# Performance work log

Hardware: AMD Instinct MI355X
Metric: run time of the kernel (lower is better)

## Reference

```python
import jax, jax.numpy as jnp
import numpy as np


def _d2(a, b):
    # squared euclidean distances, clamped at 0 (matches _full_cdist before sqrt)
    a2 = jnp.sum(a * a, axis=1)[:, None]
    b2 = jnp.sum(b * b, axis=1)[None, :]
    return jnp.clip(a2 + b2 - 2.0 * (a @ b.T), 0.0, None)


def _node_weights(pts, w1, b1, w2, b2):
    h = jax.nn.relu(pts @ w1 + b1)
    logits = h @ w2 + b2
    w = jax.nn.softplus(logits) + 1e-6
    w = w / jnp.sum(w)
    return w[:, 0]


def setup_inputs() -> dict:
    key = jax.random.key(0)
    ks = jax.random.split(key, 8)
    N, M, D, H, S = 8192, 8192, 2, 32, 3
    return {
        "base_points": jax.random.normal(ks[0], (N, D), jnp.float32),
        "target_points": jax.random.normal(ks[1], (M, D), jnp.float32),
        "log_sigmas": jnp.log(jnp.array([0.05, 0.1, 0.2], jnp.float32)),
        "log_scale": 0.1 * jax.random.normal(ks[2], (D,), jnp.float32),
        "wn_w1": jax.random.normal(ks[3], (D, H), jnp.float32) / np.sqrt(D),
        "wn_b1": jnp.zeros((H,), jnp.float32),
        "wn_w2": jax.random.normal(ks[4], (H, 1), jnp.float32) / np.sqrt(H),
        "wn_b2": jnp.zeros((1,), jnp.float32),
        "g_w1": jax.random.normal(ks[5], (4, H), jnp.float32) / 2.0,
        "g_b1": jnp.zeros((H,), jnp.float32),
        "g_w2": jax.random.normal(ks[6], (H, S), jnp.float32) / np.sqrt(H),
        "g_b2": jnp.zeros((S,), jnp.float32),
        "bias": jnp.zeros((1,), jnp.float32),
    }


def reference(base_points, target_points, log_sigmas, log_scale,
              wn_w1, wn_b1, wn_w2, wn_b2,
              g_w1, g_b1, g_w2, g_b2, bias):
    # learned anisotropic per-axis scale
    scale = jnp.exp(log_scale)
    base = base_points * scale
    target = target_points * scale

    # learned positive, normalized node weights (shared weight_net)
    w_b = _node_weights(base, wn_w1, wn_b1, wn_w2, wn_b2)
    w_t = _node_weights(target, wn_w1, wn_b1, wn_w2, wn_b2)

    # kde_mmd_loss with center=True: subtract weighted mean of each cloud.
    bc = base - jnp.sum(w_b[:, None] * base, axis=0)
    tc = target - jnp.sum(w_t[:, None] * target, axis=0)

    # squared distances computed ONCE, reused across all sigma bands
    d2_aa = _d2(bc, bc)
    d2_bb = _d2(tc, tc)
    d2_ab = _d2(bc, tc)

    sigmas = jnp.exp(log_sigmas)

    def band_loss(sigma):
        inv = 1.0 / (2.0 * sigma * sigma)
        kaa = jnp.exp(-d2_aa * inv)
        kbb = jnp.exp(-d2_bb * inv)
        kab = jnp.exp(-d2_ab * inv)
        # weighted MMD^2: w_a K_aa w_a + w_b K_bb w_b - 2 w_a K_ab w_b
        return (w_b @ (kaa @ w_b) + w_t @ (kbb @ w_t)
                - 2.0 * (w_b @ (kab @ w_t)))

    per_band = jnp.stack([band_loss(sigmas[i]) for i in range(sigmas.shape[0])])

    # gating statistics (torch.tensor([...]) detaches -> stop_gradient)
    dist = jnp.sqrt(_d2(base, target))
    mean_dist = jnp.mean(dist)
    var_dist = jnp.var(dist, ddof=1)  # torch .var() is unbiased
    n_base = base_points.shape[0]
    size_diff = abs(float(n_base - target_points.shape[0])) / (n_base + 1e-6)
    weight_var = jnp.var(w_b, ddof=1) + jnp.var(w_t, ddof=1)
    stats = jax.lax.stop_gradient(
        jnp.stack([mean_dist, var_dist,
                   jnp.asarray(size_diff, base.dtype), weight_var]))

    mix_logits = jax.nn.relu(stats @ g_w1 + g_b1) @ g_w2 + g_b2
    gw = jax.nn.softplus(mix_logits)
    gw = gw / jnp.sum(gw)
    return jnp.sum(gw * per_band) + bias[0]
```

## Files before the change

### kernel.cpp

```cpp
#include <hip/hip_runtime.h>
#include <math.h>

#define JT 64
#define ITILE 1024
#define T8 8
#define NJOB_AB 1024
#define NJOB_TRI 576
#define NBLK (NJOB_AB + 2 * NJOB_TRI)
#define L2E 1.4426950408889634f

typedef float v2f __attribute__((ext_vector_type(2)));

__device__ inline float fexp2n(float x) {
  float r;
  asm("v_exp_f32 %0, -%1" : "=v"(r) : "v"(x));
  return r;
}
__device__ inline float fsqrt(float x) {
  float r;
  asm("v_sqrt_f32 %0, %1" : "=v"(r) : "v"(x));
  return r;
}

__device__ inline double wred_d(double v) {
#pragma unroll
  for (int o = 32; o > 0; o >>= 1) v += __shfl_down(v, o, 64);
  return v;
}

__device__ inline double bred(double v, double* sm) {
  v = wred_d(v);
  __syncthreads();
  if ((threadIdx.x & 63) == 0) sm[threadIdx.x >> 6] = v;
  __syncthreads();
  return sm[0] + sm[1] + sm[2] + sm[3];
}

__device__ inline void slot_reduce(const double* slot, double* smean) {
  if (threadIdx.x < 64) {
    int l = threadIdx.x;
    const double* sl = slot + l * 4;
#pragma unroll
    for (int c = 0; c < 4; ++c) {
      double v = sl[c];
      double vb = (l < 32) ? v : 0.0;
      double vt = (l < 32) ? 0.0 : v;
      vb = wred_d(vb);
      vt = wred_d(vt);
      if (l == 0) {
        smean[c] = vb;
        smean[4 + c] = vt;
      }
    }
  }
}

__global__ __launch_bounds__(256) void prep_kernel(
    const float* __restrict__ base, const float* __restrict__ target,
    const float* __restrict__ log_sigmas, const float* __restrict__ log_scale,
    const float* __restrict__ w1, const float* __restrict__ b1,
    const float* __restrict__ w2, const float* __restrict__ b2,
    float2* __restrict__ pxy, float* __restrict__ pu,
    double* __restrict__ slot, unsigned* __restrict__ fctr, int n) {
  __shared__ double sm[4];
  int gid = blockIdx.x * 256 + threadIdx.x;
  int isT = gid >= n;
  const float* pts = isT ? target : base;
  int idx = isT ? gid - n : gid;
  float ex = __expf(log_scale[0]);
  float ey = __expf(log_scale[1]);
  float s2 = __expf(log_sigmas[2]);
  float r2 = __fsqrt_rn(L2E / (2.f * s2 * s2));
  float2 p = ((const float2*)pts)[idx];
  float xr = p.x * ex, yr = p.y * ey;
  float logit = b2[0];
#pragma unroll
  for (int k = 0; k < 32; ++k) {
    float h = fmaf(xr, w1[k], fmaf(yr, w1[32 + k], b1[k]));
    h = fmaxf(h, 0.f);
    logit = fmaf(h, w2[k], logit);
  }
  float u = fmaxf(logit, 0.f) + log1pf(__expf(-fabsf(logit))) + 1e-6f;
  float X = xr * r2, Y = yr * r2;
  pxy[gid] = make_float2(X, Y);
  pu[gid] = u;
  double su = bred((double)u, sm);
  double qu = bred((double)u * (double)u, sm);
  double mx = bred((double)u * (double)X, sm);
  double my = bred((double)u * (double)Y, sm);
  if (threadIdx.x == 0) {
    double* s = slot + blockIdx.x * 4;
    s[0] = su;
    s[1] = qu;
    s[2] = mx;
    s[3] = my;
    if (blockIdx.x == 0) *fctr = 0u;
  }
}

template <bool AB, bool FAST>
__device__ inline void tile_loop(const float* sx, const float* sy,
                                 const float* su, const float* snb,
                                 const v2f xi2[4], const v2f yi2[4],
                                 const v2f al2[4], float rr0, float rr1,
                                 v2f a0[4], v2f a1[4], v2f a2[4], float& sdo,
                                 float& sqo) {
  float sda = 0.f, sdb = 0.f;
  v2f sq2 = {0.f, 0.f};
  const v2f vz = {0.f, 0.f};
#pragma unroll 2
  for (int jj = 0; jj < JT / 2; ++jj) {
    v2f xj = *(const v2f*)&sx[2 * jj];
    v2f yj = *(const v2f*)&sy[2 * jj];
    v2f uj = *(const v2f*)&su[2 * jj];
    v2f nbj;
    if constexpr (AB) nbj = *(const v2f*)&snb[2 * jj];
#pragma unroll
    for (int i = 0; i < 4; ++i) {
      v2f dx = xi2[i] - xj;
      v2f dy = yi2[i] - yj;
      v2f pos = dx * dx + dy * dy;
      v2f k2 = {fexp2n(pos.x), fexp2n(pos.y)};
      v2f k0, k1;
      if constexpr (FAST) {
        v2f t = k2 * k2;
        k1 = t * t;
        v2f t1 = k1 * k1;
        k0 = t1 * t1;
      } else {
        v2f m1 = pos * rr1;
        v2f m0 = pos * rr0;
        k1 = {fexp2n(m1.x), fexp2n(m1.y)};
        k0 = {fexp2n(m0.x), fexp2n(m0.y)};
      }
      a0[i] += uj * k0;
      a1[i] += uj * k1;
      a2[i] += uj * k2;
      if constexpr (AB) {
        v2f anb = al2[i] + nbj;
        v2f d2u = pos + anb;
        d2u = __builtin_elementwise_max(d2u, vz);
        sq2 += d2u;
        sda += fsqrt(d2u.x);
        sdb += fsqrt(d2u.y);
      }
    }
  }
  sdo = sda + sdb;
  sqo = sq2.x + sq2.y;
}

__global__ __launch_bounds__(256) void pair_kernel(
    const float2* __restrict__ pxy, const float* __restrict__ pu,
    const double* __restrict__ slot, double* __restrict__ paa,
    double* __restrict__ pbb, double* __restrict__ pab,
    double* __restrict__ psd, double* __restrict__ psq,
    unsigned* __restrict__ fctr, const float* __restrict__ log_sigmas,
    const float* __restrict__ g_w1, const float* __restrict__ g_b1,
    const float* __restrict__ g_w2, const float* __restrict__ g_b2,
    const float* __restrict__ bias, float* __restrict__ out, int n) {
  __shared__ __align__(16) float sx[JT];
  __shared__ __align__(16) float sy[JT];
  __shared__ __align__(16) float su[JT];
  __shared__ __align__(16) float snb[JT];
  __shared__ double sm[4];
  __shared__ double smean[8];
  __shared__ int lastf;

  int b = blockIdx.x;
  int m, it, jt = 0, j0, pidx;
  if (b < NJOB_AB) {
    m = 2;
    pidx = b;
    it = b >> 7;
    j0 = (b & 127) * JT;
  } else {
    int r = b - NJOB_AB;
    m = (r < NJOB_TRI) ? 0 : 1;
    if (m == 1) r -= NJOB_TRI;
    pidx = r;
    int tile = r >> 4;
    int q = r & 15;
    int idx = tile, len = T8;
    it = 0;
    while (idx >= len) {
      idx -= len;
      --len;
      ++it;
    }
    jt = it + idx;
    j0 = jt * ITILE + q * JT;
  }
  const float2* pxyI = pxy + ((m == 1) ? n : 0);
  const float* puI = pu + ((m == 1) ? n : 0);
  const float2* pxyJ = pxy + ((m == 0) ? 0 : n);
  const float* puJ = pu + ((m == 0) ? 0 : n);

  float cx = 0.f, cy = 0.f, cx2 = 0.f, cy2 = 0.f, cc = 0.f;
  if (m == 2) {
    slot_reduce(slot, smean);
  }

  float s0 = __expf(log_sigmas[0]);
  float s1 = __expf(log_sigmas[1]);
  float s2 = __expf(log_sigmas[2]);
  float rr0 = (s2 * s2) / (s0 * s0);
  float rr1 = (s2 * s2) / (s1 * s1);
  bool fast = (fabsf(rr0 - 16.f) <= 0.016f) && (fabsf(rr1 - 4.f) <= 0.004f);

  if (m == 2) {
    __syncthreads();
    cx = (float)(smean[2] / smean[0] - smean[6] / smean[4]);
    cy = (float)(smean[3] / smean[0] - smean[7] / smean[4]);
    cx2 = 2.f * cx;
    cy2 = 2.f * cy;
    cc = cx * cx + cy * cy;
  }

  if (threadIdx.x < JT) {
    float2 v = pxyJ[j0 + threadIdx.x];
    sx[threadIdx.x] = v.x;
    sy[threadIdx.x] = v.y;
    su[threadIdx.x] = puJ[j0 + threadIdx.x];
    if (m == 2) snb[threadIdx.x] = -fmaf(cx2, v.x, cy2 * v.y);
  }
  __syncthreads();

  int i0 = it * ITILE + threadIdx.x;
  v2f xi2[4], yi2[4], al2[4];
  float u[4];
#pragma unroll
  for (int i = 0; i < 4; ++i) {
    float2 P = pxyI[i0 + i * 256];
    u[i] = puI[i0 + i * 256];
    float xv = P.x, yv = P.y, alv = 0.f;
    if (m == 2) {
      xv -= cx;
      yv -= cy;
      alv = fmaf(cx2, xv, cy2 * yv) + cc;
    }
    xi2[i] = (v2f){xv, xv};
    yi2[i] = (v2f){yv, yv};
    al2[i] = (v2f){alv, alv};
  }

  v2f a0[4] = {}, a1[4] = {}, a2[4] = {};
  float sd = 0.f, sq = 0.f;
  if (m == 2) {
    if (fast)
      tile_loop<true, true>(sx, sy, su, snb, xi2, yi2, al2, rr0, rr1, a0, a1,
                            a2, sd, sq);
    else
      tile_loop<true, false>(sx, sy, su, snb, xi2, yi2, al2, rr0, rr1, a0, a1,
                             a2, sd, sq);
  } else {
    if (fast)
      tile_loop<false, true>(sx, sy, su, snb, xi2, yi2, al2, rr0, rr1, a0, a1,
                             a2, sd, sq);
    else
      tile_loop<false, false>(sx, sy, su, snb, xi2, yi2, al2, rr0, rr1, a0,
                              a1, a2, sd, sq);
  }

  double wgt = (m != 2 && jt != it) ? 2.0 : 1.0;
  double c0 = 0.0, c1 = 0.0, c2 = 0.0;
#pragma unroll
  for (int i = 0; i < 4; ++i) {
    c0 += (double)u[i] * (double)(a0[i].x + a0[i].y);
    c1 += (double)u[i] * (double)(a1[i].x + a1[i].y);
    c2 += (double)u[i] * (double)(a2[i].x + a2[i].y);
  }
  double r0 = bred(c0, sm) * wgt;
  double r1 = bred(c1, sm) * wgt;
  double r2d = bred(c2, sm) * wgt;
  double* prow = (m == 0) ? paa : (m == 1) ? pbb : pab;
  int stride = (m == 2) ? NJOB_AB : NJOB_TRI;
  if (threadIdx.x == 0) {
    prow[0 * stride + pidx] = r0;
    prow[1 * stride + pidx] = r1;
    prow[2 * stride + pidx] = r2d;
  }
  if (m == 2) {
    double rsd = bred((double)sd, sm);
    double rsq = bred((double)sq, sm);
    if (threadIdx.x == 0) {
      psd[pidx] = rsd;
      psq[pidx] = rsq;
    }
  }

  if (threadIdx.x == 0) {
    __threadfence();
    unsigned old = atomicAdd(fctr, 1u);
    lastf = (old == NBLK - 1) ? 1 : 0;
  }
  __syncthreads();
  if (!lastf) return;
  __threadfence();

  slot_reduce(slot, smean);
  __syncthreads();
  int t = threadIdx.x;
  double vaa[3], vbb[3], vab[3];
  for (int s = 0; s < 3; ++s) {
    const double* pa = paa + s * NJOB_TRI;
    const double* pb = pbb + s * NJOB_TRI;
    const double* pc = pab + s * NJOB_AB;
    double va = pa[t] + pa[t + 256] + ((t < 64) ? pa[t + 512] : 0.0);
    double vb = pb[t] + pb[t + 256] + ((t < 64) ? pb[t + 512] : 0.0);
    double vc = pc[t] + pc[t + 256] + pc[t + 512] + pc[t + 768];
    vaa[s] = bred(va, sm);
    vbb[s] = bred(vb, sm);
    vab[s] = bred(vc, sm);
  }
  double sdt = bred(psd[t] + psd[t + 256] + psd[t + 512] + psd[t + 768], sm);
  double sqt = bred(psq[t] + psq[t + 256] + psq[t + 512] + psq[t + 768], sm);

  if (threadIdx.x == 0) {
    double Sb = smean[0], Qb = smean[1], St = smean[4], Qt = smean[5];
    double pband[3];
    for (int s = 0; s < 3; ++s)
      pband[s] = vaa[s] / (Sb * Sb) + vbb[s] / (St * St) -
                 2.0 * vab[s] / (Sb * St);
    double s2d = (double)s2;
    double r2sq = (double)L2E / (2.0 * s2d * s2d);
    double sd_real = sdt / sqrt(r2sq);
    double sq_real = sqt / r2sq;
    double NN = (double)n;
    double NM = NN * NN;
    double mean_d = sd_real / NM;
    double var_d = (sq_real - sd_real * sd_real / NM) / (NM - 1.0);
    double wv = (Qb / (Sb * Sb) - 1.0 / NN) / (NN - 1.0) +
                (Qt / (St * St) - 1.0 / NN) / (NN - 1.0);
    float st[4] = {(float)mean_d, (float)var_d, 0.f, (float)wv};
    float gl[3] = {g_b2[0], g_b2[1], g_b2[2]};
    for (int k = 0; k < 32; ++k) {
      float h = g_b1[k];
      for (int c = 0; c < 4; ++c) h = fmaf(st[c], g_w1[c * 32 + k], h);
      h = fmaxf(h, 0.f);
      for (int s = 0; s < 3; ++s) gl[s] = fmaf(h, g_w2[k * 3 + s], gl[s]);
    }
    float gw[3];
    float gsum = 0.f;
    for (int s = 0; s < 3; ++s) {
      gw[s] = fmaxf(gl[s], 0.f) + log1pf(__expf(-fabsf(gl[s])));
      gsum += gw[s];
    }
    double r = 0.0;
    for (int s = 0; s < 3; ++s) r += (double)(gw[s] / gsum) * pband[s];
    out[0] = (float)(r + (double)bias[0]);
  }
}

extern "C" void kernel_launch(void* const* d_in, const int* in_sizes, int n_in,
                              void* d_out, int out_size, void* d_ws,
                              size_t ws_size, hipStream_t stream) {
  const float* base = (const float*)d_in[0];
  const float* target = (const float*)d_in[1];
  const float* log_sigmas = (const float*)d_in[2];
  const float* log_scale = (const float*)d_in[3];
  const float* wn_w1 = (const float*)d_in[4];
  const float* wn_b1 = (const float*)d_in[5];
  const float* wn_w2 = (const float*)d_in[6];
  const float* wn_b2 = (const float*)d_in[7];
  const float* g_w1 = (const float*)d_in[8];
  const float* g_b1 = (const float*)d_in[9];
  const float* g_w2 = (const float*)d_in[10];
  const float* g_b2 = (const float*)d_in[11];
  const float* bias = (const float*)d_in[12];
  int n = in_sizes[0] / 2;

  double* dbase = (double*)d_ws;
  double* slot = dbase;
  double* paa = dbase + 256;
  double* pbb = paa + 3 * NJOB_TRI;
  double* pab = pbb + 3 * NJOB_TRI;
  double* psd = pab + 3 * NJOB_AB;
  double* psq = psd + NJOB_AB;
  double* dend = psq + NJOB_AB;
  float2* pxy = (float2*)dend;
  float* pu = (float*)(pxy + 2 * n);
  unsigned* fctr = (unsigned*)(pu + 2 * n);

  prep_kernel<<<(2 * n) / 256, 256, 0, stream>>>(
      base, target, log_sigmas, log_scale, wn_w1, wn_b1, wn_w2, wn_b2, pxy, pu,
      slot, fctr, n);
  pair_kernel<<<NBLK, 256, 0, stream>>>(pxy, pu, slot, paa, pbb, pab, psd, psq,
                                        fctr, log_sigmas, g_w1, g_b1, g_w2,
                                        g_b2, bias, (float*)d_out, n);
}
```

Before: 148.7 us.

## Expand pair distances algebraically, use packed FP32 ops, and compute squared-distance sum analytically

The inner pair loop now expands distances as |xi|^2 - 2 xi·xj + |xj|^2 using hand-written v_pk_fma/v_pk_add/v_pk_mul with op_sel broadcasts. The j-tile is packed as a float4 (x, y, |x|^2, u) in shared memory. The sum of squared cross distances is derived in closed form from per-cloud moments collected in prep, which removes the per-pair accumulation and its extra reduction. Blocks drop to 128 threads, each holding 8 i-points in packed pairs. The expanded form can lose precision through cancellation, and the closed-form sum skips the clamp at zero.

```diff
diff --git a/kernel.cpp b/kernel.cpp
--- a/kernel.cpp
+++ b/kernel.cpp
@@ -11,15 +11,58 @@
 
 typedef float v2f __attribute__((ext_vector_type(2)));
 
-__device__ inline float fexp2n(float x) {
-  float r;
-  asm("v_exp_f32 %0, -%1" : "=v"(r) : "v"(x));
-  return r;
-}
-__device__ inline float fsqrt(float x) {
-  float r;
-  asm("v_sqrt_f32 %0, %1" : "=v"(r) : "v"(x));
-  return r;
+__device__ inline v2f pk_add(v2f a, v2f b) {
+  v2f d;
+  asm("v_pk_add_f32 %0, %1, %2" : "=v"(d) : "v"(a), "v"(b));
+  return d;
+}
+__device__ inline v2f pk_mul(v2f a, v2f b) {
+  v2f d;
+  asm("v_pk_mul_f32 %0, %1, %2" : "=v"(d) : "v"(a), "v"(b));
+  return d;
+}
+__device__ inline v2f pk_fma_bh_bl(v2f a, v2f b, v2f c) {
+  v2f d;
+  asm("v_pk_fma_f32 %0, %1, %2, %3 op_sel:[0,1,0] op_sel_hi:[1,1,0]"
+      : "=v"(d) : "v"(a), "v"(b), "v"(c));
+  return d;
+}
+__device__ inline v2f pk_fma_bl(v2f a, v2f b, v2f c) {
+  v2f d;
+  asm("v_pk_fma_f32 %0, %1, %2, %3 op_sel:[0,0,0] op_sel_hi:[1,0,1]"
+      : "=v"(d) : "v"(a), "v"(b), "v"(c));
+  return d;
+}
+__device__ inline void pk_acc_bh(v2f& acc, v2f a, v2f b) {
+  asm("v_pk_fma_f32 %0, %1, %2, %0 op_sel:[0,1,0] op_sel_hi:[1,1,1]"
+      : "+v"(acc) : "v"(a), "v"(b));
+}
+__device__ inline void pk_accp(v2f& acc, v2f a) {
+  asm("v_pk_add_f32 %0, %1, %0" : "+v"(acc) : "v"(a));
+}
+__device__ inline v2f pk_add_bl(v2f a, v2f b) {
+  v2f d;
+  asm("v_pk_add_f32 %0, %1, %2 op_sel:[0,0] op_sel_hi:[1,0]"
+      : "=v"(d) : "v"(a), "v"(b));
+  return d;
+}
+__device__ inline v2f pk_add_bh(v2f a, v2f b) {
+  v2f d;
+  asm("v_pk_add_f32 %0, %1, %2 op_sel:[0,1] op_sel_hi:[1,1]"
+      : "=v"(d) : "v"(a), "v"(b));
+  return d;
+}
+__device__ inline v2f pexpn(v2f p) {
+  float lo, hi;
+  asm("v_exp_f32 %0, -%1" : "=v"(lo) : "v"(p.x));
+  asm("v_exp_f32 %0, -%1" : "=v"(hi) : "v"(p.y));
+  return (v2f){lo, hi};
+}
+__device__ inline v2f psqrta(v2f p) {
+  float lo, hi;
+  asm("v_sqrt_f32 %0, abs(%1)" : "=v"(lo) : "v"(p.x));
+  asm("v_sqrt_f32 %0, abs(%1)" : "=v"(hi) : "v"(p.y));
+  return (v2f){lo, hi};
 }
 
 __device__ inline double wred_d(double v) {
@@ -28,20 +71,23 @@
   return v;
 }
 
-__device__ inline double bred(double v, double* sm) {
+template <int NW>
+__device__ inline double bredN(double v, double* sm) {
   v = wred_d(v);
   __syncthreads();
   if ((threadIdx.x & 63) == 0) sm[threadIdx.x >> 6] = v;
   __syncthreads();
-  return sm[0] + sm[1] + sm[2] + sm[3];
-}
-
-__device__ inline void slot_reduce(const double* slot, double* smean) {
+  double r = sm[0];
+#pragma unroll
+  for (int w = 1; w < NW; ++w) r += sm[w];
+  return r;
+}
+
+__device__ inline void slot_reduce(const double* slot, double* smean, int nc) {
   if (threadIdx.x < 64) {
     int l = threadIdx.x;
-    const double* sl = slot + l * 4;
-#pragma unroll
-    for (int c = 0; c < 4; ++c) {
+    const double* sl = slot + l * 8;
+    for (int c = 0; c < nc; ++c) {
       double v = sl[c];
       double vb = (l < 32) ? v : 0.0;
       double vt = (l < 32) ? 0.0 : v;
@@ -49,7 +95,7 @@
       vt = wred_d(vt);
       if (l == 0) {
         smean[c] = vb;
-        smean[4 + c] = vt;
+        smean[8 + c] = vt;
       }
     }
   }
@@ -84,87 +130,94 @@
   float X = xr * r2, Y = yr * r2;
   pxy[gid] = make_float2(X, Y);
   pu[gid] = u;
-  double su = bred((double)u, sm);
-  double qu = bred((double)u * (double)u, sm);
-  double mx = bred((double)u * (double)X, sm);
-  double my = bred((double)u * (double)Y, sm);
+  double su = bredN<4>((double)u, sm);
+  double qu = bredN<4>((double)u * (double)u, sm);
+  double mx = bredN<4>((double)u * (double)X, sm);
+  double my = bredN<4>((double)u * (double)Y, sm);
+  double sx = bredN<4>((double)X, sm);
+  double sy = bredN<4>((double)Y, sm);
+  double sr = bredN<4>((double)X * (double)X + (double)Y * (double)Y, sm);
   if (threadIdx.x == 0) {
-    double* s = slot + blockIdx.x * 4;
+    double* s = slot + blockIdx.x * 8;
     s[0] = su;
     s[1] = qu;
     s[2] = mx;
     s[3] = my;
+    s[4] = sx;
+    s[5] = sy;
+    s[6] = sr;
+    s[7] = 0.0;
     if (blockIdx.x == 0) *fctr = 0u;
   }
 }
 
 template <bool AB, bool FAST>
-__device__ inline void tile_loop(const float* sx, const float* sy,
-                                 const float* su, const float* snb,
-                                 const v2f xi2[4], const v2f yi2[4],
-                                 const v2f al2[4], float rr0, float rr1,
-                                 v2f a0[4], v2f a1[4], v2f a2[4], float& sdo,
-                                 float& sqo) {
-  float sda = 0.f, sdb = 0.f;
-  v2f sq2 = {0.f, 0.f};
-  const v2f vz = {0.f, 0.f};
+__device__ inline void tile_loop(const float4* __restrict__ sj4,
+                                 const float* __restrict__ snb,
+                                 const v2f* xinP, const v2f* yinP,
+                                 const v2f* ricP, const v2f* ricuP,
+                                 v2f rr0p, v2f rr1p, v2f* a0, v2f* a1, v2f* a2,
+                                 v2f& sdA, v2f& sdB) {
 #pragma unroll 2
-  for (int jj = 0; jj < JT / 2; ++jj) {
-    v2f xj = *(const v2f*)&sx[2 * jj];
-    v2f yj = *(const v2f*)&sy[2 * jj];
-    v2f uj = *(const v2f*)&su[2 * jj];
-    v2f nbj;
-    if constexpr (AB) nbj = *(const v2f*)&snb[2 * jj];
-#pragma unroll
-    for (int i = 0; i < 4; ++i) {
-      v2f dx = xi2[i] - xj;
-      v2f dy = yi2[i] - yj;
-      v2f pos = dx * dx + dy * dy;
-      v2f k2 = {fexp2n(pos.x), fexp2n(pos.y)};
-      v2f k0, k1;
-      if constexpr (FAST) {
-        v2f t = k2 * k2;
-        k1 = t * t;
-        v2f t1 = k1 * k1;
-        k0 = t1 * t1;
-      } else {
-        v2f m1 = pos * rr1;
-        v2f m0 = pos * rr0;
-        k1 = {fexp2n(m1.x), fexp2n(m1.y)};
-        k0 = {fexp2n(m0.x), fexp2n(m0.y)};
+  for (int j2 = 0; j2 < JT / 2; ++j2) {
+    float4 q0 = sj4[2 * j2];
+    float4 q1 = sj4[2 * j2 + 1];
+    v2f nbp;
+    if constexpr (AB) nbp = *(const v2f*)&snb[2 * j2];
+#pragma unroll
+    for (int h = 0; h < 2; ++h) {
+      float4 q = h ? q1 : q0;
+      v2f xy = (v2f){q.x, q.y};
+      v2f ru = (v2f){q.z, q.w};
+#pragma unroll
+      for (int k = 0; k < 4; ++k) {
+        v2f c = pk_fma_bh_bl(yinP[k], xy, ru);
+        c = pk_fma_bl(xinP[k], xy, c);
+        v2f pos = pk_add(c, ricP[k]);
+        v2f e = pexpn(pos);
+        pk_acc_bh(a2[k], e, ru);
+        if constexpr (FAST) {
+          v2f t = pk_mul(e, e);
+          v2f k1v = pk_mul(t, t);
+          pk_acc_bh(a1[k], k1v, ru);
+          v2f t1 = pk_mul(k1v, k1v);
+          v2f k0v = pk_mul(t1, t1);
+          pk_acc_bh(a0[k], k0v, ru);
+        } else {
+          v2f m1 = pk_mul(pos, rr1p);
+          v2f m0 = pk_mul(pos, rr0p);
+          v2f e1 = pexpn(m1);
+          pk_acc_bh(a1[k], e1, ru);
+          v2f e0 = pexpn(m0);
+          pk_acc_bh(a0[k], e0, ru);
+        }
+        if constexpr (AB) {
+          v2f du = pk_add(c, ricuP[k]);
+          du = h ? pk_add_bh(du, nbp) : pk_add_bl(du, nbp);
+          v2f s = psqrta(du);
+          if (k & 2)
+            pk_accp(sdB, s);
+          else
+            pk_accp(sdA, s);
+        }
       }
-      a0[i] += uj * k0;
-      a1[i] += uj * k1;
-      a2[i] += uj * k2;
-      if constexpr (AB) {
-        v2f anb = al2[i] + nbj;
-        v2f d2u = pos + anb;
-        d2u = __builtin_elementwise_max(d2u, vz);
-        sq2 += d2u;
-        sda += fsqrt(d2u.x);
-        sdb += fsqrt(d2u.y);
-      }
-    }
-  }
-  sdo = sda + sdb;
-  sqo = sq2.x + sq2.y;
-}
-
-__global__ __launch_bounds__(256) void pair_kernel(
+    }
+  }
+}
+
+__global__ __launch_bounds__(128) void pair_kernel(
     const float2* __restrict__ pxy, const float* __restrict__ pu,
     const double* __restrict__ slot, double* __restrict__ paa,
     double* __restrict__ pbb, double* __restrict__ pab,
-    double* __restrict__ psd, double* __restrict__ psq,
-    unsigned* __restrict__ fctr, const float* __restrict__ log_sigmas,
-    const float* __restrict__ g_w1, const float* __restrict__ g_b1,
-    const float* __restrict__ g_w2, const float* __restrict__ g_b2,
-    const float* __restrict__ bias, float* __restrict__ out, int n) {
-  __shared__ __align__(16) float sx[JT];
-  __shared__ __align__(16) float sy[JT];
-  __shared__ __align__(16) float su[JT];
+    double* __restrict__ psd, unsigned* __restrict__ fctr,
+    const float* __restrict__ log_sigmas, const float* __restrict__ g_w1,
+    const float* __restrict__ g_b1, const float* __restrict__ g_w2,
+    const float* __restrict__ g_b2, const float* __restrict__ bias,
+    float* __restrict__ out, int n) {
+  __shared__ __align__(16) float4 sj4[JT];
   __shared__ __align__(16) float snb[JT];
-  __shared__ double sm[4];
-  __shared__ double smean[8];
+  __shared__ double sm[2];
+  __shared__ double smean[16];
   __shared__ int lastf;
 
   int b = blockIdx.x;
@@ -198,7 +251,7 @@
 
   float cx = 0.f, cy = 0.f, cx2 = 0.f, cy2 = 0.f, cc = 0.f;
   if (m == 2) {
-    slot_reduce(slot, smean);
+    slot_reduce(slot, smean, 4);
   }
 
   float s0 = __expf(log_sigmas[0]);
@@ -207,11 +260,12 @@
   float rr0 = (s2 * s2) / (s0 * s0);
   float rr1 = (s2 * s2) / (s1 * s1);
   bool fast = (fabsf(rr0 - 16.f) <= 0.016f) && (fabsf(rr1 - 4.f) <= 0.004f);
+  v2f rr0p = (v2f){rr0, rr0}, rr1p = (v2f){rr1, rr1};
 
   if (m == 2) {
     __syncthreads();
-    cx = (float)(smean[2] / smean[0] - smean[6] / smean[4]);
-    cy = (float)(smean[3] / smean[0] - smean[7] / smean[4]);
+    cx = (float)(smean[2] / smean[0] - smean[10] / smean[8]);
+    cy = (float)(smean[3] / smean[0] - smean[11] / smean[8]);
     cx2 = 2.f * cx;
     cy2 = 2.f * cy;
     cc = cx * cx + cy * cy;
@@ -219,60 +273,68 @@
 
   if (threadIdx.x < JT) {
     float2 v = pxyJ[j0 + threadIdx.x];
-    sx[threadIdx.x] = v.x;
-    sy[threadIdx.x] = v.y;
-    su[threadIdx.x] = puJ[j0 + threadIdx.x];
+    float uu = puJ[j0 + threadIdx.x];
+    float r = fmaf(v.x, v.x, v.y * v.y);
+    sj4[threadIdx.x] = make_float4(v.x, v.y, r, uu);
     if (m == 2) snb[threadIdx.x] = -fmaf(cx2, v.x, cy2 * v.y);
   }
   __syncthreads();
 
   int i0 = it * ITILE + threadIdx.x;
-  v2f xi2[4], yi2[4], al2[4];
-  float u[4];
-#pragma unroll
-  for (int i = 0; i < 4; ++i) {
-    float2 P = pxyI[i0 + i * 256];
-    u[i] = puI[i0 + i * 256];
-    float xv = P.x, yv = P.y, alv = 0.f;
+  v2f xinP[4], yinP[4], ricP[4], ricuP[4];
+#pragma unroll
+  for (int k = 0; k < 4; ++k) {
+    float2 P0 = pxyI[i0 + (2 * k) * 128];
+    float2 P1 = pxyI[i0 + (2 * k + 1) * 128];
+    float x0 = P0.x, y0 = P0.y, x1 = P1.x, y1 = P1.y;
+    float al0 = 0.f, al1 = 0.f;
     if (m == 2) {
-      xv -= cx;
-      yv -= cy;
-      alv = fmaf(cx2, xv, cy2 * yv) + cc;
-    }
-    xi2[i] = (v2f){xv, xv};
-    yi2[i] = (v2f){yv, yv};
-    al2[i] = (v2f){alv, alv};
+      x0 -= cx;
+      y0 -= cy;
+      x1 -= cx;
+      y1 -= cy;
+      al0 = fmaf(cx2, x0, cy2 * y0) + cc;
+      al1 = fmaf(cx2, x1, cy2 * y1) + cc;
+    }
+    xinP[k] = (v2f){-2.f * x0, -2.f * x1};
+    yinP[k] = (v2f){-2.f * y0, -2.f * y1};
+    float r0 = fmaf(x0, x0, y0 * y0);
+    float r1 = fmaf(x1, x1, y1 * y1);
+    ricP[k] = (v2f){r0, r1};
+    ricuP[k] = (v2f){r0 + al0, r1 + al1};
   }
 
   v2f a0[4] = {}, a1[4] = {}, a2[4] = {};
-  float sd = 0.f, sq = 0.f;
+  v2f sdA = (v2f){0.f, 0.f}, sdB = (v2f){0.f, 0.f};
   if (m == 2) {
     if (fast)
-      tile_loop<true, true>(sx, sy, su, snb, xi2, yi2, al2, rr0, rr1, a0, a1,
-                            a2, sd, sq);
+      tile_loop<true, true>(sj4, snb, xinP, yinP, ricP, ricuP, rr0p, rr1p, a0,
+                            a1, a2, sdA, sdB);
     else
-      tile_loop<true, false>(sx, sy, su, snb, xi2, yi2, al2, rr0, rr1, a0, a1,
-                             a2, sd, sq);
+      tile_loop<true, false>(sj4, snb, xinP, yinP, ricP, ricuP, rr0p, rr1p, a0,
+                             a1, a2, sdA, sdB);
   } else {
     if (fast)
-      tile_loop<false, true>(sx, sy, su, snb, xi2, yi2, al2, rr0, rr1, a0, a1,
-                             a2, sd, sq);
+      tile_loop<false, true>(sj4, snb, xinP, yinP, ricP, ricuP, rr0p, rr1p, a0,
+                             a1, a2, sdA, sdB);
     else
-      tile_loop<false, false>(sx, sy, su, snb, xi2, yi2, al2, rr0, rr1, a0,
-                              a1, a2, sd, sq);
+      tile_loop<false, false>(sj4, snb, xinP, yinP, ricP, ricuP, rr0p, rr1p,
+                              a0, a1, a2, sdA, sdB);
   }
 
   double wgt = (m != 2 && jt != it) ? 2.0 : 1.0;
   double c0 = 0.0, c1 = 0.0, c2 = 0.0;
 #pragma unroll
-  for (int i = 0; i < 4; ++i) {
-    c0 += (double)u[i] * (double)(a0[i].x + a0[i].y);
-    c1 += (double)u[i] * (double)(a1[i].x + a1[i].y);
-    c2 += (double)u[i] * (double)(a2[i].x + a2[i].y);
-  }
-  double r0 = bred(c0, sm) * wgt;
-  double r1 = bred(c1, sm) * wgt;
-  double r2d = bred(c2, sm) * wgt;
+  for (int k = 0; k < 4; ++k) {
+    double u0 = (double)puI[i0 + (2 * k) * 128];
+    double u1 = (double)puI[i0 + (2 * k + 1) * 128];
+    c0 += u0 * (double)a0[k].x + u1 * (double)a0[k].y;
+    c1 += u0 * (double)a1[k].x + u1 * (double)a1[k].y;
+    c2 += u0 * (double)a2[k].x + u1 * (double)a2[k].y;
+  }
+  double r0 = bredN<2>(c0, sm) * wgt;
+  double r1 = bredN<2>(c1, sm) * wgt;
+  double r2d = bredN<2>(c2, sm) * wgt;
   double* prow = (m == 0) ? paa : (m == 1) ? pbb : pab;
   int stride = (m == 2) ? NJOB_AB : NJOB_TRI;
   if (threadIdx.x == 0) {
@@ -281,12 +343,9 @@
     prow[2 * stride + pidx] = r2d;
   }
   if (m == 2) {
-    double rsd = bred((double)sd, sm);
-    double rsq = bred((double)sq, sm);
-    if (threadIdx.x == 0) {
-      psd[pidx] = rsd;
-      psq[pidx] = rsq;
-    }
+    float sd = sdA.x + sdA.y + sdB.x + sdB.y;
+    double rsd = bredN<2>((double)sd, sm);
+    if (threadIdx.x == 0) psd[pidx] = rsd;
   }
 
   if (threadIdx.x == 0) {
@@ -298,7 +357,7 @@
   if (!lastf) return;
   __threadfence();
 
-  slot_reduce(slot, smean);
+  slot_reduce(slot, smean, 7);
   __syncthreads();
   int t = threadIdx.x;
   double vaa[3], vbb[3], vab[3];
@@ -306,27 +365,36 @@
     const double* pa = paa + s * NJOB_TRI;
     const double* pb = pbb + s * NJOB_TRI;
     const double* pc = pab + s * NJOB_AB;
-    double va = pa[t] + pa[t + 256] + ((t < 64) ? pa[t + 512] : 0.0);
-    double vb = pb[t] + pb[t + 256] + ((t < 64) ? pb[t + 512] : 0.0);
-    double vc = pc[t] + pc[t + 256] + pc[t + 512] + pc[t + 768];
-    vaa[s] = bred(va, sm);
-    vbb[s] = bred(vb, sm);
-    vab[s] = bred(vc, sm);
-  }
-  double sdt = bred(psd[t] + psd[t + 256] + psd[t + 512] + psd[t + 768], sm);
-  double sqt = bred(psq[t] + psq[t + 256] + psq[t + 512] + psq[t + 768], sm);
+    double va = pa[t] + pa[t + 128] + pa[t + 256] + pa[t + 384] +
+                ((t < 64) ? pa[t + 512] : 0.0);
+    double vb = pb[t] + pb[t + 128] + pb[t + 256] + pb[t + 384] +
+                ((t < 64) ? pb[t + 512] : 0.0);
+    double vc = 0.0;
+#pragma unroll
+    for (int qq = 0; qq < 8; ++qq) vc += pc[t + 128 * qq];
+    vaa[s] = bredN<2>(va, sm);
+    vbb[s] = bredN<2>(vb, sm);
+    vab[s] = bredN<2>(vc, sm);
+  }
+  double sdv = 0.0;
+#pragma unroll
+  for (int qq = 0; qq < 8; ++qq) sdv += psd[t + 128 * qq];
+  double sdt = bredN<2>(sdv, sm);
 
   if (threadIdx.x == 0) {
-    double Sb = smean[0], Qb = smean[1], St = smean[4], Qt = smean[5];
+    double Sb = smean[0], Qb = smean[1], St = smean[8], Qt = smean[9];
+    double SXb = smean[4], SYb = smean[5], SRb = smean[6];
+    double SXt = smean[12], SYt = smean[13], SRt = smean[14];
     double pband[3];
     for (int s = 0; s < 3; ++s)
       pband[s] = vaa[s] / (Sb * Sb) + vbb[s] / (St * St) -
                  2.0 * vab[s] / (Sb * St);
+    double NN = (double)n;
+    double sq_sc = NN * (SRb + SRt) - 2.0 * (SXb * SXt + SYb * SYt);
     double s2d = (double)s2;
     double r2sq = (double)L2E / (2.0 * s2d * s2d);
     double sd_real = sdt / sqrt(r2sq);
-    double sq_real = sqt / r2sq;
-    double NN = (double)n;
+    double sq_real = sq_sc / r2sq;
     double NM = NN * NN;
     double mean_d = sd_real / NM;
     double var_d = (sq_real - sd_real * sd_real / NM) / (NM - 1.0);
@@ -372,12 +440,11 @@
 
   double* dbase = (double*)d_ws;
   double* slot = dbase;
-  double* paa = dbase + 256;
+  double* paa = dbase + 512;
   double* pbb = paa + 3 * NJOB_TRI;
   double* pab = pbb + 3 * NJOB_TRI;
   double* psd = pab + 3 * NJOB_AB;
-  double* psq = psd + NJOB_AB;
-  double* dend = psq + NJOB_AB;
+  double* dend = psd + NJOB_AB;
   float2* pxy = (float2*)dend;
   float* pu = (float*)(pxy + 2 * n);
   unsigned* fctr = (unsigned*)(pu + 2 * n);
@@ -385,7 +452,7 @@
   prep_kernel<<<(2 * n) / 256, 256, 0, stream>>>(
       base, target, log_sigmas, log_scale, wn_w1, wn_b1, wn_w2, wn_b2, pxy, pu,
       slot, fctr, n);
-  pair_kernel<<<NBLK, 256, 0, stream>>>(pxy, pu, slot, paa, pbb, pab, psd, psq,
+  pair_kernel<<<NBLK, 128, 0, stream>>>(pxy, pu, slot, paa, pbb, pab, psd,
                                         fctr, log_sigmas, g_w1, g_b1, g_w2,
                                         g_b2, bias, (float*)d_out, n);
 }
```

New measurement: 159.1 us. 1.07x slower.

## Compute distance sum-of-squares in closed form and halve AB job tile width

Applied to the files above, without the earlier changes.

The per-pair sum of squared base-target distances is now derived analytically from per-cloud sums of X, Y and X²+Y², which prep computes. This removes the per-pair accumulation and its reduction from the AB inner loop. AB jobs also now use a 32-wide j-tile, doubling the AB block count for better load balance across the grid. The tradeoffs are more blocks with less work each, three extra block reductions in prep, and possible precision loss, because the closed form subtracts large double terms instead of applying the per-pair zero clamp.

```diff
diff --git a/kernel.cpp b/kernel.cpp
--- a/kernel.cpp
+++ b/kernel.cpp
@@ -1,10 +1,11 @@
 #include <hip/hip_runtime.h>
 #include <math.h>
 
-#define JT 64
+#define JTA 32
+#define JTT 64
 #define ITILE 1024
 #define T8 8
-#define NJOB_AB 1024
+#define NJOB_AB 2048
 #define NJOB_TRI 576
 #define NBLK (NJOB_AB + 2 * NJOB_TRI)
 #define L2E 1.4426950408889634f
@@ -36,12 +37,11 @@
   return sm[0] + sm[1] + sm[2] + sm[3];
 }
 
-__device__ inline void slot_reduce(const double* slot, double* smean) {
+__device__ inline void slot_reduce(const double* slot, double* smean, int nc) {
   if (threadIdx.x < 64) {
     int l = threadIdx.x;
-    const double* sl = slot + l * 4;
-#pragma unroll
-    for (int c = 0; c < 4; ++c) {
+    const double* sl = slot + l * 8;
+    for (int c = 0; c < nc; ++c) {
       double v = sl[c];
       double vb = (l < 32) ? v : 0.0;
       double vt = (l < 32) ? 0.0 : v;
@@ -49,7 +49,7 @@
       vt = wred_d(vt);
       if (l == 0) {
         smean[c] = vb;
-        smean[4 + c] = vt;
+        smean[8 + c] = vt;
       }
     }
   }
@@ -88,12 +88,19 @@
   double qu = bred((double)u * (double)u, sm);
   double mx = bred((double)u * (double)X, sm);
   double my = bred((double)u * (double)Y, sm);
+  double sx = bred((double)X, sm);
+  double sy = bred((double)Y, sm);
+  double sr = bred((double)X * (double)X + (double)Y * (double)Y, sm);
   if (threadIdx.x == 0) {
-    double* s = slot + blockIdx.x * 4;
+    double* s = slot + blockIdx.x * 8;
     s[0] = su;
     s[1] = qu;
     s[2] = mx;
     s[3] = my;
+    s[4] = sx;
+    s[5] = sy;
+    s[6] = sr;
+    s[7] = 0.0;
     if (blockIdx.x == 0) *fctr = 0u;
   }
 }
@@ -103,13 +110,12 @@
                                  const float* su, const float* snb,
                                  const v2f xi2[4], const v2f yi2[4],
                                  const v2f al2[4], float rr0, float rr1,
-                                 v2f a0[4], v2f a1[4], v2f a2[4], float& sdo,
-                                 float& sqo) {
+                                 v2f a0[4], v2f a1[4], v2f a2[4], float& sdo) {
+  constexpr int N2 = (AB ? JTA : JTT) / 2;
   float sda = 0.f, sdb = 0.f;
-  v2f sq2 = {0.f, 0.f};
   const v2f vz = {0.f, 0.f};
 #pragma unroll 2
-  for (int jj = 0; jj < JT / 2; ++jj) {
+  for (int jj = 0; jj < N2; ++jj) {
     v2f xj = *(const v2f*)&sx[2 * jj];
     v2f yj = *(const v2f*)&sy[2 * jj];
     v2f uj = *(const v2f*)&su[2 * jj];
@@ -140,31 +146,29 @@
         v2f anb = al2[i] + nbj;
         v2f d2u = pos + anb;
         d2u = __builtin_elementwise_max(d2u, vz);
-        sq2 += d2u;
         sda += fsqrt(d2u.x);
         sdb += fsqrt(d2u.y);
       }
     }
   }
   sdo = sda + sdb;
-  sqo = sq2.x + sq2.y;
 }
 
 __global__ __launch_bounds__(256) void pair_kernel(
     const float2* __restrict__ pxy, const float* __restrict__ pu,
     const double* __restrict__ slot, double* __restrict__ paa,
     double* __restrict__ pbb, double* __restrict__ pab,
-    double* __restrict__ psd, double* __restrict__ psq,
-    unsigned* __restrict__ fctr, const float* __restrict__ log_sigmas,
-    const float* __restrict__ g_w1, const float* __restrict__ g_b1,
-    const float* __restrict__ g_w2, const float* __restrict__ g_b2,
-    const float* __restrict__ bias, float* __restrict__ out, int n) {
-  __shared__ __align__(16) float sx[JT];
-  __shared__ __align__(16) float sy[JT];
-  __shared__ __align__(16) float su[JT];
-  __shared__ __align__(16) float snb[JT];
+    double* __restrict__ psd, unsigned* __restrict__ fctr,
+    const float* __restrict__ log_sigmas, const float* __restrict__ g_w1,
+    const float* __restrict__ g_b1, const float* __restrict__ g_w2,
+    const float* __restrict__ g_b2, const float* __restrict__ bias,
+    float* __restrict__ out, int n) {
+  __shared__ __align__(16) float sx[JTT];
+  __shared__ __align__(16) float sy[JTT];
+  __shared__ __align__(16) float su[JTT];
+  __shared__ __align__(16) float snb[JTT];
   __shared__ double sm[4];
-  __shared__ double smean[8];
+  __shared__ double smean[16];
   __shared__ int lastf;
 
   int b = blockIdx.x;
@@ -172,8 +176,8 @@
   if (b < NJOB_AB) {
     m = 2;
     pidx = b;
-    it = b >> 7;
-    j0 = (b & 127) * JT;
+    it = b >> 8;
+    j0 = (b & 255) * JTA;
   } else {
     int r = b - NJOB_AB;
     m = (r < NJOB_TRI) ? 0 : 1;
@@ -189,7 +193,7 @@
       ++it;
     }
     jt = it + idx;
-    j0 = jt * ITILE + q * JT;
+    j0 = jt * ITILE + q * JTT;
   }
   const float2* pxyI = pxy + ((m == 1) ? n : 0);
   const float* puI = pu + ((m == 1) ? n : 0);
@@ -198,7 +202,7 @@
 
   float cx = 0.f, cy = 0.f, cx2 = 0.f, cy2 = 0.f, cc = 0.f;
   if (m == 2) {
-    slot_reduce(slot, smean);
+    slot_reduce(slot, smean, 4);
   }
 
   float s0 = __expf(log_sigmas[0]);
@@ -210,14 +214,15 @@
 
   if (m == 2) {
     __syncthreads();
-    cx = (float)(smean[2] / smean[0] - smean[6] / smean[4]);
-    cy = (float)(smean[3] / smean[0] - smean[7] / smean[4]);
+    cx = (float)(smean[2] / smean[0] - smean[10] / smean[8]);
+    cy = (float)(smean[3] / smean[0] - smean[11] / smean[8]);
     cx2 = 2.f * cx;
     cy2 = 2.f * cy;
     cc = cx * cx + cy * cy;
   }
 
-  if (threadIdx.x < JT) {
+  int jcnt = (m == 2) ? JTA : JTT;
+  if (threadIdx.x < jcnt) {
     float2 v = pxyJ[j0 + threadIdx.x];
     sx[threadIdx.x] = v.x;
     sy[threadIdx.x] = v.y;
@@ -245,21 +250,21 @@
   }
 
   v2f a0[4] = {}, a1[4] = {}, a2[4] = {};
-  float sd = 0.f, sq = 0.f;
+  float sd = 0.f;
   if (m == 2) {
     if (fast)
       tile_loop<true, true>(sx, sy, su, snb, xi2, yi2, al2, rr0, rr1, a0, a1,
-                            a2, sd, sq);
+                            a2, sd);
     else
       tile_loop<true, false>(sx, sy, su, snb, xi2, yi2, al2, rr0, rr1, a0, a1,
-                             a2, sd, sq);
+                             a2, sd);
   } else {
     if (fast)
       tile_loop<false, true>(sx, sy, su, snb, xi2, yi2, al2, rr0, rr1, a0, a1,
-                             a2, sd, sq);
+                             a2, sd);
     else
       tile_loop<false, false>(sx, sy, su, snb, xi2, yi2, al2, rr0, rr1, a0,
-                              a1, a2, sd, sq);
+                              a1, a2, sd);
   }
 
   double wgt = (m != 2 && jt != it) ? 2.0 : 1.0;
@@ -282,11 +287,7 @@
   }
   if (m == 2) {
     double rsd = bred((double)sd, sm);
-    double rsq = bred((double)sq, sm);
-    if (threadIdx.x == 0) {
-      psd[pidx] = rsd;
-      psq[pidx] = rsq;
-    }
+    if (threadIdx.x == 0) psd[pidx] = rsd;
   }
 
   if (threadIdx.x == 0) {
@@ -298,7 +299,7 @@
   if (!lastf) return;
   __threadfence();
 
-  slot_reduce(slot, smean);
+  slot_reduce(slot, smean, 7);
   __syncthreads();
   int t = threadIdx.x;
   double vaa[3], vbb[3], vab[3];
@@ -308,25 +309,32 @@
     const double* pc = pab + s * NJOB_AB;
     double va = pa[t] + pa[t + 256] + ((t < 64) ? pa[t + 512] : 0.0);
     double vb = pb[t] + pb[t + 256] + ((t < 64) ? pb[t + 512] : 0.0);
-    double vc = pc[t] + pc[t + 256] + pc[t + 512] + pc[t + 768];
+    double vc = 0.0;
+#pragma unroll
+    for (int qq = 0; qq < 8; ++qq) vc += pc[t + 256 * qq];
     vaa[s] = bred(va, sm);
     vbb[s] = bred(vb, sm);
     vab[s] = bred(vc, sm);
   }
-  double sdt = bred(psd[t] + psd[t + 256] + psd[t + 512] + psd[t + 768], sm);
-  double sqt = bred(psq[t] + psq[t + 256] + psq[t + 512] + psq[t + 768], sm);
+  double sdv = 0.0;
+#pragma unroll
+  for (int qq = 0; qq < 8; ++qq) sdv += psd[t + 256 * qq];
+  double sdt = bred(sdv, sm);
 
   if (threadIdx.x == 0) {
-    double Sb = smean[0], Qb = smean[1], St = smean[4], Qt = smean[5];
+    double Sb = smean[0], Qb = smean[1], St = smean[8], Qt = smean[9];
+    double SXb = smean[4], SYb = smean[5], SRb = smean[6];
+    double SXt = smean[12], SYt = smean[13], SRt = smean[14];
     double pband[3];
     for (int s = 0; s < 3; ++s)
       pband[s] = vaa[s] / (Sb * Sb) + vbb[s] / (St * St) -
                  2.0 * vab[s] / (Sb * St);
+    double NN = (double)n;
+    double sq_sc = NN * (SRb + SRt) - 2.0 * (SXb * SXt + SYb * SYt);
     double s2d = (double)s2;
     double r2sq = (double)L2E / (2.0 * s2d * s2d);
     double sd_real = sdt / sqrt(r2sq);
-    double sq_real = sqt / r2sq;
-    double NN = (double)n;
+    double sq_real = sq_sc / r2sq;
     double NM = NN * NN;
     double mean_d = sd_real / NM;
     double var_d = (sq_real - sd_real * sd_real / NM) / (NM - 1.0);
@@ -372,12 +380,11 @@
 
   double* dbase = (double*)d_ws;
   double* slot = dbase;
-  double* paa = dbase + 256;
+  double* paa = dbase + 512;
   double* pbb = paa + 3 * NJOB_TRI;
   double* pab = pbb + 3 * NJOB_TRI;
   double* psd = pab + 3 * NJOB_AB;
-  double* psq = psd + NJOB_AB;
-  double* dend = psq + NJOB_AB;
+  double* dend = psd + NJOB_AB;
   float2* pxy = (float2*)dend;
   float* pu = (float*)(pxy + 2 * n);
   unsigned* fctr = (unsigned*)(pu + 2 * n);
@@ -385,7 +392,7 @@
   prep_kernel<<<(2 * n) / 256, 256, 0, stream>>>(
       base, target, log_sigmas, log_scale, wn_w1, wn_b1, wn_w2, wn_b2, pxy, pu,
       slot, fctr, n);
-  pair_kernel<<<NBLK, 256, 0, stream>>>(pxy, pu, slot, paa, pbb, pab, psd, psq,
+  pair_kernel<<<NBLK, 256, 0, stream>>>(pxy, pu, slot, paa, pbb, pab, psd,
                                         fctr, log_sigmas, g_w1, g_b1, g_w2,
                                         g_b2, bias, (float*)d_out, n);
 }
```

Measured after the change: 166.0 us. 11.7% more time.
